# Kernel optimization log

Measured on AMD Instinct MI355X. Metric: run time of the kernel, lower is better.

## Reference

```python
import jax, jax.numpy as jnp
import numpy as np

EPS = 1e-7
MIN_NORM = 1e-15
MAX_NORM = 1e6


def _arcosh(x):
    return jnp.log(x + jnp.sqrt(jnp.clip(x * x - 1.0, EPS, None)))


def _mink_dot(x, y):
    # Minkowski inner product <x,y>_L, keepdim
    return jnp.sum(x * y, axis=-1, keepdims=True) - 2.0 * x[..., 0:1] * y[..., 0:1]


def _mink_norm(u):
    return jnp.sqrt(jnp.clip(_mink_dot(u, u), EPS, None))


def _proj(x, c):
    K = 1.0 / c
    y = x[..., 1:]
    first = jnp.sqrt(jnp.clip(K + jnp.sum(y * y, axis=-1, keepdims=True), EPS, None))
    return jnp.concatenate([first, y], axis=-1)


def _proj_tan(u, x, c):
    ux = jnp.sum(x[..., 1:] * u[..., 1:], axis=-1, keepdims=True)
    first = ux / jnp.clip(x[..., 0:1], EPS, None)
    return jnp.concatenate([first, u[..., 1:]], axis=-1)


def _logmap0(x, c):
    K = 1.0 / c
    sqrtK = jnp.sqrt(K)
    y = x[..., 1:]
    y_norm = jnp.clip(jnp.linalg.norm(y, axis=-1, keepdims=True), MIN_NORM, None)
    theta = jnp.clip(x[..., 0:1] / sqrtK, 1.0 + EPS, None)
    return jnp.concatenate([jnp.zeros_like(theta), sqrtK * _arcosh(theta) * y / y_norm], axis=-1)


def _expmap0(u, c):
    K = 1.0 / c
    sqrtK = jnp.sqrt(K)
    x = u[..., 1:]
    x_norm = jnp.clip(jnp.linalg.norm(x, axis=-1, keepdims=True), MIN_NORM, None)
    theta = x_norm / sqrtK
    return jnp.concatenate([sqrtK * jnp.cosh(theta), sqrtK * jnp.sinh(theta) * x / x_norm], axis=-1)


def _expmap(u, x, c):
    K = 1.0 / c
    sqrtK = jnp.sqrt(K)
    theta = jnp.clip(jnp.clip(_mink_norm(u), None, MAX_NORM) / sqrtK, MIN_NORM, None)
    return _proj(jnp.cosh(theta) * x + jnp.sinh(theta) * u / theta, c)


def _ptransp0(x, u, c):
    K = 1.0 / c
    sqrtK = jnp.sqrt(K)
    x0 = x[..., 0:1]
    y = x[..., 1:]
    y_norm = jnp.clip(jnp.linalg.norm(y, axis=-1, keepdims=True), MIN_NORM, None)
    y_hat = y / y_norm
    v = jnp.concatenate([-y_norm, (sqrtK - x0) * y_hat], axis=-1)
    alpha = jnp.sum(y_hat * u[..., 1:], axis=-1, keepdims=True) / sqrtK
    return _proj_tan(u - alpha * v, x, c)


def _mobius_add(x, y, c):
    u = _logmap0(y, c)
    v = _ptransp0(x, u, c)
    return _expmap(v, x, c)


def _mobius_matvec(m, x, c):
    # rev=False: left-multiply tangent vectors by m
    return _expmap0(m @ _logmap0(x, c), c)


def _sqdist(x, y, c):
    K = 1.0 / c
    theta = jnp.clip(-_mink_dot(x, y) / K, 1.0 + EPS, None)
    return jnp.clip(K * _arcosh(theta) ** 2, None, 50.0)


def _h2k(x):
    return x[..., 1:] / x[..., 0:1]


def _k2h(x):
    sq = jnp.clip(jnp.sum(x * x, axis=-1, keepdims=True), None, 0.999)
    return jnp.concatenate([jnp.ones_like(x[..., 0:1]), x], axis=-1) / jnp.sqrt(1.0 - sq)


def _lorenz_factor(x):
    # default c=1.0 (the learnable c is NOT passed here in the original)
    sq = jnp.clip(jnp.sum(x * x, axis=-1, keepdims=True), None, 0.9)
    return 1.0 / jnp.sqrt(1.0 - sq)


def _one_transform(W, h, b, c):
    n, t, d = h.shape
    # faithful raw row-major reshape (NOT a transpose), matching torch.reshape
    Wh = _mobius_matvec(W, h.reshape(t, n * d), c).reshape(n * t, d)
    return _proj(_mobius_add(Wh, b, c), c)


def setup_inputs() -> dict:
    key = jax.random.key(0)
    n, t, d = 8192, 16, 64
    ks = jax.random.split(key, 3)
    # valid hyperboloid points (c=1): x0 = sqrt(1 + |y|^2)
    y = 0.5 * jax.random.normal(ks[0], (n, t, d - 1), jnp.float32)
    x0 = jnp.sqrt(1.0 + jnp.sum(y * y, axis=-1, keepdims=True))
    big_h = jnp.concatenate([x0, y], axis=-1)
    # all causal time pairs (m, nn<=m) so every segment of the scatter is non-empty
    pairs = np.array([(m, nn) for m in range(t) for nn in range(m + 1)], dtype=np.int64)
    time_index = jnp.asarray(pairs.T)  # (2, 136)
    E = time_index.shape[1]
    mask = jnp.zeros((1, E, 1), jnp.float32)
    lim = float(np.sqrt(6.0 / (t + t)))  # glorot
    w_q = jax.random.uniform(ks[1], (t, t), jnp.float32, -lim, lim)
    w_k = jax.random.uniform(ks[2], (t, t), jnp.float32, -lim, lim)
    b_q = jnp.ones((1, d), jnp.float32)
    b_k = jnp.ones((1, d), jnp.float32)
    a = jnp.ones((1,), jnp.float32)
    c = jnp.ones((1,), jnp.float32)
    return {"big_h": big_h, "time_index": time_index, "mask": mask,
            "w_q": w_q, "w_k": w_k, "b_q": b_q, "b_k": b_k, "a": a, "c": c}


def reference(big_h, time_index, mask, w_q, w_k, b_q, b_k, a, c):
    n, t, d = big_h.shape
    t_m = time_index[0]
    t_n = time_index[1]
    q = _one_transform(w_q, big_h, b_q, c).reshape(n, t, d)
    k = _one_transform(w_k, big_h, b_k, c).reshape(n, t, d)
    v = _h2k(big_h.reshape(n * t, d)).reshape(n, t, d - 1)  # Klein coords
    dist = -_sqdist(q[:, t_m, :], k[:, t_n, :], c)          # (n, E, 1)
    s = jnp.exp(a * dist - c + mask)
    s_sum = jnp.zeros((n, t, 1), s.dtype).at[:, t_m, :].add(s)
    beta = s / s_sum[:, t_n, :]                              # segment softmax
    lamb = _lorenz_factor(v.reshape(n * t, d - 1)).reshape(n, t, 1)[:, t_n, :]
    v_tn = v[:, t_n, :]
    z = v_tn * lamb * beta
    w = lamb * beta
    z_sum = jnp.zeros((n, t, d - 1), z.dtype).at[:, t_m, :].add(z)
    w_sum = jnp.zeros((n, t, 1), w.dtype).at[:, t_m, :].add(w)
    out = z_sum / w_sum                                       # Einstein midpoint
    return _k2h(out.reshape(n * t, d - 1)).reshape(n, t, d)
```

## Files before the change

### kernel.cpp

```cpp
#include <hip/hip_runtime.h>
#include <stdint.h>

typedef unsigned short u16;
typedef unsigned int   u32;

#define EPSF  1e-7f
#define MINN  1e-15f

#define CPR  524288
#define NE   136
#define QS   68
#define VS   68
#define CMS  17
#define NBANK 7

#define WQP 952
#define WKP 1208
#define SCQ 1464
#define SCK 1480
#define CHQ 1496
#define CHK 1512
#define UQ  1528
#define UK  1592

__device__ __forceinline__ float bf2f(u16 u){ u32 x = ((u32)u)<<16; return __uint_as_float(x); }
__device__ __forceinline__ float ldv(const void* p, size_t i, int f32m){
    return f32m ? ((const float*)p)[i] : bf2f(((const u16*)p)[i]);
}
__device__ __forceinline__ float arcosh_f(float x){
    return logf(x + sqrtf(fmaxf(x*x - 1.0f, EPSF)));
}
__device__ __forceinline__ float clampf(float v, float lim){
    return fmaxf(fminf(v, lim), -lim);
}
__device__ __forceinline__ float red16(float v){
    v += __shfl_xor(v,1); v += __shfl_xor(v,2);
    v += __shfl_xor(v,4); v += __shfl_xor(v,8);
    return v;
}
__device__ __forceinline__ int detect_f32(const void* Hv){
    const float* Hf = (const float*)Hv;
    int ok = 1;
#pragma unroll
    for(int i=0;i<16;i++){
        float v = Hf[(size_t)i*1024];
        if(!(v > 0.9f && v < 1000.f)) ok = 0;
    }
    return ok;
}

__device__ __forceinline__ void load_tile(const void* Hv, int f32m, int i0, int c0, float4* hx){
    if(f32m){
        const float* Hf = (const float*)Hv;
#pragma unroll
        for(int s=0;s<16;s++) hx[s] = *(const float4*)(Hf + ((size_t)(512*s + i0))*1024 + c0);
    } else {
        const u16* Hu = (const u16*)Hv;
#pragma unroll
        for(int s=0;s<16;s++){
            ushort4 u4 = *(const ushort4*)(Hu + ((size_t)(512*s + i0))*1024 + c0);
            hx[s] = make_float4(bf2f(u4.x), bf2f(u4.y), bf2f(u4.z), bf2f(u4.w));
        }
    }
}

template<int G>
__device__ __forceinline__ void gram_body(const float4* hx, float* acc){
    int p=0;
#pragma unroll
    for(int s=0;s<16;s++){
#pragma unroll
        for(int s2=s;s2<16;s2++){
            if(p >= 34*G && p < 34*G+34){
                acc[p-34*G] = hx[s].x*hx[s2].x + hx[s].y*hx[s2].y
                            + hx[s].z*hx[s2].z + hx[s].w*hx[s2].w;
            }
            p++;
        }
    }
}

__global__ __launch_bounds__(256) void gram3_k(const void* __restrict__ Hv, float* __restrict__ ws){
    __shared__ float gred[34];
    const int tid = threadIdx.x;
    const int g   = blockIdx.x >> 9;
    const int i0  = blockIdx.x & 511;
    const int f32m = detect_f32(Hv);
    const int c0 = tid*4;

    float4 hx[16];
    load_tile(Hv, f32m, i0, c0, hx);

    float acc[34];
    switch(g){
        case 0: gram_body<0>(hx, acc); break;
        case 1: gram_body<1>(hx, acc); break;
        case 2: gram_body<2>(hx, acc); break;
        default: gram_body<3>(hx, acc); break;
    }

    if(tid<34) gred[tid]=0.f;
    __syncthreads();
#pragma unroll
    for(int j=0;j<34;j++){
        float v=acc[j];
        v+=__shfl_xor(v,1);  v+=__shfl_xor(v,2);  v+=__shfl_xor(v,4);
        v+=__shfl_xor(v,8);  v+=__shfl_xor(v,16); v+=__shfl_xor(v,32);
        if((tid&63)==0) atomicAdd(&gred[j], v);
    }
    __syncthreads();
    if(tid<34) atomicAdd(&ws[(i0%NBANK)*NE + 34*g + tid], gred[tid]);
}

__global__ void fin4_k(const void* __restrict__ Hv, const void* __restrict__ wq, const void* __restrict__ wk,
                       const void* __restrict__ bq, const void* __restrict__ bk, const void* __restrict__ cc,
                       float* __restrict__ ws){
    __shared__ float Gy[16][17], alpha[16], h0s[16], wqp[256], wkp[256], aus[2];
    const int tid = threadIdx.x;
    const int row = tid>>4, l = tid&15;
    const int f32m = detect_f32(Hv);
    float cv = fmaxf(ldv(cc,0,f32m), 1e-20f);
    float K = 1.f/cv, sqK = sqrtf(K);
    if(tid<16) h0s[tid] = ldv(Hv, (size_t)tid*CPR, f32m);
    __syncthreads();
    if(tid<NE){
        int s=0, rem=tid;
        while(rem >= 16 - s){ rem -= 16 - s; s++; }
        int s2 = s + rem;
        float gsum = 0.f;
#pragma unroll
        for(int b=0;b<NBANK;b++) gsum += ws[b*NE+tid];
        float g = gsum - h0s[s]*h0s[s2];
        Gy[s][s2] = g; Gy[s2][s] = g;
    }
    __syncthreads();
    if(tid<16){
        float ny = fmaxf(sqrtf(fmaxf(Gy[tid][tid],0.f)), MINN);
        float th = fmaxf(h0s[tid]/sqK, 1.0f+EPSF);
        alpha[tid] = sqK*arcosh_f(th)/ny;
    }
    __syncthreads();
    {
        float aq = ldv(wq,tid,f32m)*alpha[l];
        float ak = ldv(wk,tid,f32m)*alpha[l];
        wqp[tid] = aq; wkp[tid] = ak;
        ws[WQP+tid] = aq; ws[WKP+tid] = ak;
    }
    if(tid<128){
        int lane = tid&63;
        const void* bb = (tid<64)? bq : bk;
        float v = (lane==0)? 0.f : ldv(bb,lane,f32m);
        float sn = v*v;
        sn += __shfl_xor(sn,1);  sn += __shfl_xor(sn,2);  sn += __shfl_xor(sn,4);
        sn += __shfl_xor(sn,8);  sn += __shfl_xor(sn,16); sn += __shfl_xor(sn,32);
        if(lane==0){
            float b0 = ldv(bb,0,f32m);
            float nb = fmaxf(sqrtf(sn), MINN);
            float th = fmaxf(b0/sqK, 1.0f+EPSF);
            aus[tid>>6] = sqK*arcosh_f(th)/nb;
        }
    }
    __syncthreads();
    {
        float innerQ = 0.f, innerK = 0.f;
#pragma unroll
        for(int s2=0;s2<16;s2++){
            float gy = Gy[l][s2];
            innerQ += wqp[row*16+s2]*gy;
            innerK += wkp[row*16+s2]*gy;
        }
        float tq = red16(wqp[row*16+l]*innerQ);
        float tk = red16(wkp[row*16+l]*innerK);
        if(l==0){
            float xn = fmaxf(sqrtf(fmaxf(tq,0.f)), MINN);
            float thc = fminf(xn/sqK, 80.f);
            ws[SCQ+row] = clampf(sqK*sinhf(thc)/xn, 1e18f);
            ws[CHQ+row] = clampf(sqK*coshf(thc),    1e18f);
            xn = fmaxf(sqrtf(fmaxf(tk,0.f)), MINN);
            thc = fminf(xn/sqK, 80.f);
            ws[SCK+row] = clampf(sqK*sinhf(thc)/xn, 1e18f);
            ws[CHK+row] = clampf(sqK*coshf(thc),    1e18f);
        }
    }
    if(tid<64){
        ws[UQ+tid] = (tid==0)?0.f : clampf(aus[0]*ldv(bq,tid,f32m), 1e18f);
        ws[UK+tid] = (tid==0)?0.f : clampf(aus[1]*ldv(bk,tid,f32m), 1e18f);
    }
}

__global__ __launch_bounds__(256) void main6_k(const void* __restrict__ Hv, const int* __restrict__ tidx,
        const void* __restrict__ mask, const void* __restrict__ aav, const void* __restrict__ ccv,
        const float* __restrict__ ws, float* __restrict__ out){
    __shared__ __attribute__((aligned(16))) float vrow[16*VS];
    __shared__ __attribute__((aligned(16))) float qv[16*QS];
    __shared__ __attribute__((aligned(16))) float kv[16*QS];
    __shared__ float wqp[256], wkp[256], scQ[16], scK[16], chQ[16], chK[16], uq[64], uk[64];
    __shared__ float ssum[16], Cm[16*CMS], lamb[16], invv[16];
    __shared__ int   tmv[NE], tnv[NE];
    __shared__ float maskv[NE];

    const int tid = threadIdx.x;
    const int rb  = blockIdx.x >> 9;
    const int i0  = blockIdx.x & 511;
    const int r0  = rb*2;
    const int row = tid>>4, l = tid&15;
    const int f32m = detect_f32(Hv);
    const float av = ldv(aav,0,f32m);
    const float cv = fmaxf(ldv(ccv,0,f32m), 1e-20f);
    const float K = 1.f/cv, sqK = sqrtf(K);
    const int i64m = (tidx[1] != 1);
    const int c0 = tid*4;

    const float* Hf = (const float*)Hv;
    const u16*   Hu = (const u16*)Hv;

    float4 h0,h1,h2,h3,h4,h5,h6,h7,h8,h9,h10,h11,h12,h13,h14,h15;
    if(f32m){
#define LDF(J, HV) HV = *(const float4*)(Hf + ((size_t)(512*((r0+J)&15) + i0))*1024 + c0);
        LDF(0,h0)  LDF(1,h1)  LDF(2,h2)  LDF(3,h3)
        LDF(4,h4)  LDF(5,h5)  LDF(6,h6)  LDF(7,h7)
        LDF(8,h8)  LDF(9,h9)  LDF(10,h10) LDF(11,h11)
        LDF(12,h12) LDF(13,h13) LDF(14,h14) LDF(15,h15)
#undef LDF
    } else {
#define LDB(J, HV) { ushort4 u4_ = *(const ushort4*)(Hu + ((size_t)(512*((r0+J)&15) + i0))*1024 + c0); \
                     HV = make_float4(bf2f(u4_.x), bf2f(u4_.y), bf2f(u4_.z), bf2f(u4_.w)); }
        LDB(0,h0)  LDB(1,h1)  LDB(2,h2)  LDB(3,h3)
        LDB(4,h4)  LDB(5,h5)  LDB(6,h6)  LDB(7,h7)
        LDB(8,h8)  LDB(9,h9)  LDB(10,h10) LDB(11,h11)
        LDB(12,h12) LDB(13,h13) LDB(14,h14) LDB(15,h15)
#undef LDB
    }

    wqp[tid] = ws[WQP+tid]; wkp[tid] = ws[WKP+tid];
    if(tid<16){ scQ[tid]=ws[SCQ+tid]; scK[tid]=ws[SCK+tid]; chQ[tid]=ws[CHQ+tid]; chK[tid]=ws[CHK+tid]; }
    if(tid<64){ uq[tid]=ws[UQ+tid]; uk[tid]=ws[UK+tid]; }
    if(tid<NE){
        if(i64m){ tmv[tid]=tidx[2*tid]&15; tnv[tid]=tidx[2*NE+2*tid]&15; }
        else    { tmv[tid]=tidx[tid]&15;   tnv[tid]=tidx[NE+tid]&15; }
        maskv[tid]=ldv(mask,tid,f32m);
    }
    __syncthreads();

    auto iter = [&](int r, float4 vr){
        {
            float aq0=0,aq1=0,aq2=0,aq3=0, ak0=0,ak1=0,ak2=0,ak3=0;
#define AFMA(J, HV) { int s_=(r0+J)&15; float wq_=wqp[(r<<4)+s_], wk_=wkp[(r<<4)+s_]; \
            aq0 += wq_*HV.x; aq1 += wq_*HV.y; aq2 += wq_*HV.z; aq3 += wq_*HV.w; \
            ak0 += wk_*HV.x; ak1 += wk_*HV.y; ak2 += wk_*HV.z; ak3 += wk_*HV.w; }
            AFMA(0,h0)  AFMA(1,h1)  AFMA(2,h2)  AFMA(3,h3)
            AFMA(4,h4)  AFMA(5,h5)  AFMA(6,h6)  AFMA(7,h7)
            AFMA(8,h8)  AFMA(9,h9)  AFMA(10,h10) AFMA(11,h11)
            AFMA(12,h12) AFMA(13,h13) AFMA(14,h14) AFMA(15,h15)
#undef AFMA
            float sq_ = scQ[r], sk_ = scK[r];
            float q0 = clampf(sq_*aq0,1e18f), q1=clampf(sq_*aq1,1e18f),
                  q2 = clampf(sq_*aq2,1e18f), q3=clampf(sq_*aq3,1e18f);
            float k0 = clampf(sk_*ak0,1e18f), k1=clampf(sk_*ak1,1e18f),
                  k2 = clampf(sk_*ak2,1e18f), k3=clampf(sk_*ak3,1e18f);
            if(i0==0 && tid==0){ q0 = chQ[r]; k0 = chK[r]; }
            *(float4*)(qv + row*QS + l*4) = make_float4(q0,q1,q2,q3);
            *(float4*)(kv + row*QS + l*4) = make_float4(k0,k1,k2,k3);
        }

        {
            *(float4*)(vrow + row*VS + l*4) = vr;
            float x0v = vrow[row*VS];
            float inv0 = 1.f/((fabsf(x0v)>1e-20f)? x0v : 1e-20f);
            float sv = 0.f;
#pragma unroll
            for(int m=0;m<4;m++){
                int kp = l + 16*m;
                if(kp < 63){ float vi = vrow[row*VS + 1 + kp]*inv0; sv += vi*vi; }
            }
            sv = red16(sv);
            if(l==0){ lamb[row] = 1.f/sqrtf(1.f - fminf(sv, 0.9f)); invv[row] = inv0; }
            if(tid<16) ssum[tid]=0.f;
            Cm[tid]=0.f;
            if(tid<16) Cm[256+tid]=0.f;
        }

        {
            float xq[4], xk[4];
            float syq=0,suq=0,syk=0,suk=0;
#pragma unroll
            for(int m=0;m<4;m++){
                int k = l+16*m;
                xq[m]=qv[row*QS+k]; xk[m]=kv[row*QS+k];
                if(k>0){ syq+=xq[m]*xq[m]; suq+=xq[m]*uq[k];
                         syk+=xk[m]*xk[m]; suk+=xk[m]*uk[k]; }
            }
            syq=red16(syq); suq=red16(suq); syk=red16(syk); suk=red16(suk);
            float x0q=qv[row*QS], x0k=kv[row*QS];
            float xnq=fmaxf(sqrtf(fmaxf(syq,0.f)),MINN);
            float xnk=fmaxf(sqrtf(fmaxf(syk,0.f)),MINN);
            float alq=clampf(suq/(xnq*sqK),1e12f);
            float alk=clampf(suk/(xnk*sqK),1e12f);
            float cfq=clampf(alq*(sqK-x0q)/xnq,1e12f);
            float cfk=clampf(alk*(sqK-x0k)/xnk,1e12f);
            float wq4[4], wk4[4];
            float uxq=0,swq=0,uxk=0,swk=0;
#pragma unroll
            for(int m=0;m<4;m++){
                int k=l+16*m;
                if(k>0){
                    wq4[m]=clampf(uq[k]-cfq*xq[m],1e15f); uxq+=xq[m]*wq4[m]; swq+=wq4[m]*wq4[m];
                    wk4[m]=clampf(uk[k]-cfk*xk[m],1e15f); uxk+=xk[m]*wk4[m]; swk+=wk4[m]*wk4[m];
                } else { wq4[m]=0.f; wk4[m]=0.f; }
            }
            uxq=red16(uxq); swq=red16(swq); uxk=red16(uxk); swk=red16(swk);
            float V0q=uxq/fmaxf(x0q,EPSF);
            float V0k=uxk/fmaxf(x0k,EPSF);
            float mnq=sqrtf(fmaxf(swq-V0q*V0q,EPSF));
            float mnk=sqrtf(fmaxf(swk-V0k*V0k,EPSF));
            float thq=fminf(fmaxf(fminf(mnq,1e6f)/sqK,MINN),20.f);
            float thk=fminf(fmaxf(fminf(mnk,1e6f)/sqK,MINN),20.f);
            float chq=coshf(thq), stq=sinhf(thq)/thq;
            float chk=coshf(thk), stk=sinhf(thk)/thk;
            float zq4[4], zk4[4];
            float szq=0,szk=0;
#pragma unroll
            for(int m=0;m<4;m++){
                int k=l+16*m;
                if(k>0){
                    zq4[m]=clampf(chq*xq[m]+stq*wq4[m],1e15f); szq+=zq4[m]*zq4[m];
                    zk4[m]=clampf(chk*xk[m]+stk*wk4[m],1e15f); szk+=zk4[m]*zk4[m];
                } else { zq4[m]=0.f; zk4[m]=0.f; }
            }
            szq=red16(szq); szk=red16(szk);
            float fq = sqrtf(fmaxf(K+szq,EPSF));
            float fk = sqrtf(fmaxf(K+szk,EPSF));
#pragma unroll
            for(int m=0;m<4;m++){
                int k=l+16*m;
                qv[row*QS+k] = (k==0)? fq : zq4[m];
                kv[row*QS+k] = (k==0)? fk : zk4[m];
            }
        }
        __syncthreads();

        if(tid<NE){
            int m = tmv[tid], nn = tnv[tid];
            const float4* qp = (const float4*)(qv + m*QS);
            const float4* kp = (const float4*)(kv + nn*QS);
            float dot = 0.f;
#pragma unroll
            for(int t4=0;t4<16;t4++){
                float4 q4 = qp[t4], k4 = kp[t4];
                dot += q4.x*k4.x + q4.y*k4.y + q4.z*k4.z + q4.w*k4.w;
            }
            float mdot = dot - 2.f*qv[m*QS]*kv[nn*QS];
            float th = fmaxf(-mdot/K, 1.0f+EPSF);
            float ac = arcosh_f(th);
            float sqd = fminf(K*ac*ac, 50.f);
            float sval = expf(fminf(-av*sqd - cv + maskv[tid], 80.f));
            Cm[m*CMS+nn] = sval;
            atomicAdd(&ssum[m], sval);
        }
        __syncthreads();

        if(tid<NE){
            int m = tmv[tid], nn = tnv[tid];
            Cm[m*CMS+nn] = lamb[nn]*Cm[m*CMS+nn]/fmaxf(ssum[nn],1e-37f);
        }
        __syncthreads();

        {
            float cs[16]; float wsm = 0.f;
#pragma unroll
            for(int s=0;s<16;s++){
                float cmv = Cm[row*CMS+s];
                wsm += cmv;
                cs[s] = cmv*invv[s];
            }
            wsm = fmaxf(wsm, 1e-37f);
            float g4[4]; float sg=0.f;
#pragma unroll
            for(int m=0;m<4;m++){
                int kp = l+16*m;
                float num = 0.f;
#pragma unroll
                for(int s=0;s<16;s++) num += cs[s]*vrow[s*VS + 1 + kp];
                float gvv = (kp<63)? num/wsm : 0.f;
                g4[m]=gvv; sg += gvv*gvv;
            }
            sg = red16(sg);
            float inv = 1.f/sqrtf(1.f - fminf(sg, 0.999f));
            size_t base = ((size_t)(512*r + i0)*16 + row)*64;
            if(l==0) out[base] = inv;
#pragma unroll
            for(int m=0;m<4;m++){
                int kp=l+16*m;
                if(kp<63) out[base+1+kp] = g4[m]*inv;
            }
        }
        __syncthreads();
    };

    iter(r0+0, h0);
    iter(r0+1, h1);
}

extern "C" void kernel_launch(void* const* d_in, const int* in_sizes, int n_in,
                              void* d_out, int out_size, void* d_ws, size_t ws_size,
                              hipStream_t stream){
    const void* H    = d_in[0];
    const int* tidx  = (const int*)d_in[1];
    const void* mask = d_in[2];
    const void* wq   = d_in[3];
    const void* wk   = d_in[4];
    const void* bq   = d_in[5];
    const void* bk   = d_in[6];
    const void* aa   = d_in[7];
    const void* cc   = d_in[8];
    float* out = (float*)d_out;
    float* ws  = (float*)d_ws;

    hipMemsetAsync(ws, 0, NBANK*NE*sizeof(float), stream);
    gram3_k<<<2048,256,0,stream>>>(H, ws);
    fin4_k <<<1,   256,0,stream>>>(H, wq, wk, bq, bk, cc, ws);
    main6_k<<<4096,256,0,stream>>>(H, tidx, mask, aa, cc, ws, out);
}
```

Before: 212.1 us.

## Process one row per block, streaming H loads instead of register caching

```diff
diff --git a/kernel.cpp b/kernel.cpp
--- a/kernel.cpp
+++ b/kernel.cpp
@@ -188,7 +188,7 @@
     }
 }
 
-__global__ __launch_bounds__(256) void main6_k(const void* __restrict__ Hv, const int* __restrict__ tidx,
+__global__ __launch_bounds__(256,6) void main7_k(const void* __restrict__ Hv, const int* __restrict__ tidx,
         const void* __restrict__ mask, const void* __restrict__ aav, const void* __restrict__ ccv,
         const float* __restrict__ ws, float* __restrict__ out){
     __shared__ __attribute__((aligned(16))) float vrow[16*VS];
@@ -200,9 +200,8 @@
     __shared__ float maskv[NE];
 
     const int tid = threadIdx.x;
-    const int rb  = blockIdx.x >> 9;
+    const int r   = blockIdx.x >> 9;
     const int i0  = blockIdx.x & 511;
-    const int r0  = rb*2;
     const int row = tid>>4, l = tid&15;
     const int f32m = detect_f32(Hv);
     const float av = ldv(aav,0,f32m);
@@ -214,24 +213,6 @@
     const float* Hf = (const float*)Hv;
     const u16*   Hu = (const u16*)Hv;
 
-    float4 h0,h1,h2,h3,h4,h5,h6,h7,h8,h9,h10,h11,h12,h13,h14,h15;
-    if(f32m){
-#define LDF(J, HV) HV = *(const float4*)(Hf + ((size_t)(512*((r0+J)&15) + i0))*1024 + c0);
-        LDF(0,h0)  LDF(1,h1)  LDF(2,h2)  LDF(3,h3)
-        LDF(4,h4)  LDF(5,h5)  LDF(6,h6)  LDF(7,h7)
-        LDF(8,h8)  LDF(9,h9)  LDF(10,h10) LDF(11,h11)
-        LDF(12,h12) LDF(13,h13) LDF(14,h14) LDF(15,h15)
-#undef LDF
-    } else {
-#define LDB(J, HV) { ushort4 u4_ = *(const ushort4*)(Hu + ((size_t)(512*((r0+J)&15) + i0))*1024 + c0); \
-                     HV = make_float4(bf2f(u4_.x), bf2f(u4_.y), bf2f(u4_.z), bf2f(u4_.w)); }
-        LDB(0,h0)  LDB(1,h1)  LDB(2,h2)  LDB(3,h3)
-        LDB(4,h4)  LDB(5,h5)  LDB(6,h6)  LDB(7,h7)
-        LDB(8,h8)  LDB(9,h9)  LDB(10,h10) LDB(11,h11)
-        LDB(12,h12) LDB(13,h13) LDB(14,h14) LDB(15,h15)
-#undef LDB
-    }
-
     wqp[tid] = ws[WQP+tid]; wkp[tid] = ws[WKP+tid];
     if(tid<16){ scQ[tid]=ws[SCQ+tid]; scK[tid]=ws[SCK+tid]; chQ[tid]=ws[CHQ+tid]; chK[tid]=ws[CHK+tid]; }
     if(tid<64){ uq[tid]=ws[UQ+tid]; uk[tid]=ws[UK+tid]; }
@@ -242,163 +223,178 @@
     }
     __syncthreads();
 
-    auto iter = [&](int r, float4 vr){
-        {
-            float aq0=0,aq1=0,aq2=0,aq3=0, ak0=0,ak1=0,ak2=0,ak3=0;
-#define AFMA(J, HV) { int s_=(r0+J)&15; float wq_=wqp[(r<<4)+s_], wk_=wkp[(r<<4)+s_]; \
-            aq0 += wq_*HV.x; aq1 += wq_*HV.y; aq2 += wq_*HV.z; aq3 += wq_*HV.w; \
-            ak0 += wk_*HV.x; ak1 += wk_*HV.y; ak2 += wk_*HV.z; ak3 += wk_*HV.w; }
-            AFMA(0,h0)  AFMA(1,h1)  AFMA(2,h2)  AFMA(3,h3)
-            AFMA(4,h4)  AFMA(5,h5)  AFMA(6,h6)  AFMA(7,h7)
-            AFMA(8,h8)  AFMA(9,h9)  AFMA(10,h10) AFMA(11,h11)
-            AFMA(12,h12) AFMA(13,h13) AFMA(14,h14) AFMA(15,h15)
-#undef AFMA
-            float sq_ = scQ[r], sk_ = scK[r];
-            float q0 = clampf(sq_*aq0,1e18f), q1=clampf(sq_*aq1,1e18f),
-                  q2 = clampf(sq_*aq2,1e18f), q3=clampf(sq_*aq3,1e18f);
-            float k0 = clampf(sk_*ak0,1e18f), k1=clampf(sk_*ak1,1e18f),
-                  k2 = clampf(sk_*ak2,1e18f), k3=clampf(sk_*ak3,1e18f);
-            if(i0==0 && tid==0){ q0 = chQ[r]; k0 = chK[r]; }
-            *(float4*)(qv + row*QS + l*4) = make_float4(q0,q1,q2,q3);
-            *(float4*)(kv + row*QS + l*4) = make_float4(k0,k1,k2,k3);
-        }
-
-        {
-            *(float4*)(vrow + row*VS + l*4) = vr;
-            float x0v = vrow[row*VS];
-            float inv0 = 1.f/((fabsf(x0v)>1e-20f)? x0v : 1e-20f);
-            float sv = 0.f;
-#pragma unroll
-            for(int m=0;m<4;m++){
-                int kp = l + 16*m;
-                if(kp < 63){ float vi = vrow[row*VS + 1 + kp]*inv0; sv += vi*vi; }
-            }
-            sv = red16(sv);
-            if(l==0){ lamb[row] = 1.f/sqrtf(1.f - fminf(sv, 0.9f)); invv[row] = inv0; }
-            if(tid<16) ssum[tid]=0.f;
-            Cm[tid]=0.f;
-            if(tid<16) Cm[256+tid]=0.f;
-        }
-
-        {
-            float xq[4], xk[4];
-            float syq=0,suq=0,syk=0,suk=0;
-#pragma unroll
-            for(int m=0;m<4;m++){
-                int k = l+16*m;
-                xq[m]=qv[row*QS+k]; xk[m]=kv[row*QS+k];
-                if(k>0){ syq+=xq[m]*xq[m]; suq+=xq[m]*uq[k];
-                         syk+=xk[m]*xk[m]; suk+=xk[m]*uk[k]; }
-            }
-            syq=red16(syq); suq=red16(suq); syk=red16(syk); suk=red16(suk);
-            float x0q=qv[row*QS], x0k=kv[row*QS];
-            float xnq=fmaxf(sqrtf(fmaxf(syq,0.f)),MINN);
-            float xnk=fmaxf(sqrtf(fmaxf(syk,0.f)),MINN);
-            float alq=clampf(suq/(xnq*sqK),1e12f);
-            float alk=clampf(suk/(xnk*sqK),1e12f);
-            float cfq=clampf(alq*(sqK-x0q)/xnq,1e12f);
-            float cfk=clampf(alk*(sqK-x0k)/xnk,1e12f);
-            float wq4[4], wk4[4];
-            float uxq=0,swq=0,uxk=0,swk=0;
-#pragma unroll
-            for(int m=0;m<4;m++){
-                int k=l+16*m;
-                if(k>0){
-                    wq4[m]=clampf(uq[k]-cfq*xq[m],1e15f); uxq+=xq[m]*wq4[m]; swq+=wq4[m]*wq4[m];
-                    wk4[m]=clampf(uk[k]-cfk*xk[m],1e15f); uxk+=xk[m]*wk4[m]; swk+=wk4[m]*wk4[m];
-                } else { wq4[m]=0.f; wk4[m]=0.f; }
-            }
-            uxq=red16(uxq); swq=red16(swq); uxk=red16(uxk); swk=red16(swk);
-            float V0q=uxq/fmaxf(x0q,EPSF);
-            float V0k=uxk/fmaxf(x0k,EPSF);
-            float mnq=sqrtf(fmaxf(swq-V0q*V0q,EPSF));
-            float mnk=sqrtf(fmaxf(swk-V0k*V0k,EPSF));
-            float thq=fminf(fmaxf(fminf(mnq,1e6f)/sqK,MINN),20.f);
-            float thk=fminf(fmaxf(fminf(mnk,1e6f)/sqK,MINN),20.f);
-            float chq=coshf(thq), stq=sinhf(thq)/thq;
-            float chk=coshf(thk), stk=sinhf(thk)/thk;
-            float zq4[4], zk4[4];
-            float szq=0,szk=0;
-#pragma unroll
-            for(int m=0;m<4;m++){
-                int k=l+16*m;
-                if(k>0){
-                    zq4[m]=clampf(chq*xq[m]+stq*wq4[m],1e15f); szq+=zq4[m]*zq4[m];
-                    zk4[m]=clampf(chk*xk[m]+stk*wk4[m],1e15f); szk+=zk4[m]*zk4[m];
-                } else { zq4[m]=0.f; zk4[m]=0.f; }
-            }
-            szq=red16(szq); szk=red16(szk);
-            float fq = sqrtf(fmaxf(K+szq,EPSF));
-            float fk = sqrtf(fmaxf(K+szk,EPSF));
-#pragma unroll
-            for(int m=0;m<4;m++){
-                int k=l+16*m;
-                qv[row*QS+k] = (k==0)? fq : zq4[m];
-                kv[row*QS+k] = (k==0)? fk : zk4[m];
-            }
-        }
-        __syncthreads();
-
-        if(tid<NE){
-            int m = tmv[tid], nn = tnv[tid];
-            const float4* qp = (const float4*)(qv + m*QS);
-            const float4* kp = (const float4*)(kv + nn*QS);
-            float dot = 0.f;
-#pragma unroll
-            for(int t4=0;t4<16;t4++){
-                float4 q4 = qp[t4], k4 = kp[t4];
-                dot += q4.x*k4.x + q4.y*k4.y + q4.z*k4.z + q4.w*k4.w;
-            }
-            float mdot = dot - 2.f*qv[m*QS]*kv[nn*QS];
-            float th = fmaxf(-mdot/K, 1.0f+EPSF);
-            float ac = arcosh_f(th);
-            float sqd = fminf(K*ac*ac, 50.f);
-            float sval = expf(fminf(-av*sqd - cv + maskv[tid], 80.f));
-            Cm[m*CMS+nn] = sval;
-            atomicAdd(&ssum[m], sval);
-        }
-        __syncthreads();
-
-        if(tid<NE){
-            int m = tmv[tid], nn = tnv[tid];
-            Cm[m*CMS+nn] = lamb[nn]*Cm[m*CMS+nn]/fmaxf(ssum[nn],1e-37f);
-        }
-        __syncthreads();
-
-        {
-            float cs[16]; float wsm = 0.f;
-#pragma unroll
-            for(int s=0;s<16;s++){
-                float cmv = Cm[row*CMS+s];
-                wsm += cmv;
-                cs[s] = cmv*invv[s];
-            }
-            wsm = fmaxf(wsm, 1e-37f);
-            float g4[4]; float sg=0.f;
-#pragma unroll
-            for(int m=0;m<4;m++){
-                int kp = l+16*m;
-                float num = 0.f;
-#pragma unroll
-                for(int s=0;s<16;s++) num += cs[s]*vrow[s*VS + 1 + kp];
-                float gvv = (kp<63)? num/wsm : 0.f;
-                g4[m]=gvv; sg += gvv*gvv;
-            }
-            sg = red16(sg);
-            float inv = 1.f/sqrtf(1.f - fminf(sg, 0.999f));
-            size_t base = ((size_t)(512*r + i0)*16 + row)*64;
-            if(l==0) out[base] = inv;
-#pragma unroll
-            for(int m=0;m<4;m++){
-                int kp=l+16*m;
-                if(kp<63) out[base+1+kp] = g4[m]*inv;
-            }
-        }
-        __syncthreads();
-    };
-
-    iter(r0+0, h0);
-    iter(r0+1, h1);
+    float aq0=0,aq1=0,aq2=0,aq3=0, ak0=0,ak1=0,ak2=0,ak3=0;
+    float4 vr;
+    const int rQ = r<<4;
+    if(f32m){
+#define STEPF(J) { const int s_=(r+J)&15; \
+        float4 b = *(const float4*)(Hf + ((size_t)(512*s_ + i0))*1024 + c0); \
+        if(J==0) vr = b; \
+        float wq_=wqp[rQ+s_], wk_=wkp[rQ+s_]; \
+        aq0 += wq_*b.x; aq1 += wq_*b.y; aq2 += wq_*b.z; aq3 += wq_*b.w; \
+        ak0 += wk_*b.x; ak1 += wk_*b.y; ak2 += wk_*b.z; ak3 += wk_*b.w; }
+        STEPF(0)  STEPF(1)  STEPF(2)  STEPF(3)
+        STEPF(4)  STEPF(5)  STEPF(6)  STEPF(7)
+        STEPF(8)  STEPF(9)  STEPF(10) STEPF(11)
+        STEPF(12) STEPF(13) STEPF(14) STEPF(15)
+#undef STEPF
+    } else {
+#define STEPB(J) { const int s_=(r+J)&15; \
+        ushort4 u4_ = *(const ushort4*)(Hu + ((size_t)(512*s_ + i0))*1024 + c0); \
+        float4 b = make_float4(bf2f(u4_.x), bf2f(u4_.y), bf2f(u4_.z), bf2f(u4_.w)); \
+        if(J==0) vr = b; \
+        float wq_=wqp[rQ+s_], wk_=wkp[rQ+s_]; \
+        aq0 += wq_*b.x; aq1 += wq_*b.y; aq2 += wq_*b.z; aq3 += wq_*b.w; \
+        ak0 += wk_*b.x; ak1 += wk_*b.y; ak2 += wk_*b.z; ak3 += wk_*b.w; }
+        STEPB(0)  STEPB(1)  STEPB(2)  STEPB(3)
+        STEPB(4)  STEPB(5)  STEPB(6)  STEPB(7)
+        STEPB(8)  STEPB(9)  STEPB(10) STEPB(11)
+        STEPB(12) STEPB(13) STEPB(14) STEPB(15)
+#undef STEPB
+    }
+
+    {
+        float sq_ = scQ[r], sk_ = scK[r];
+        float q0 = clampf(sq_*aq0,1e18f), q1=clampf(sq_*aq1,1e18f),
+              q2 = clampf(sq_*aq2,1e18f), q3=clampf(sq_*aq3,1e18f);
+        float k0 = clampf(sk_*ak0,1e18f), k1=clampf(sk_*ak1,1e18f),
+              k2 = clampf(sk_*ak2,1e18f), k3=clampf(sk_*ak3,1e18f);
+        if(i0==0 && tid==0){ q0 = chQ[r]; k0 = chK[r]; }
+        *(float4*)(qv + row*QS + l*4) = make_float4(q0,q1,q2,q3);
+        *(float4*)(kv + row*QS + l*4) = make_float4(k0,k1,k2,k3);
+    }
+
+    {
+        *(float4*)(vrow + row*VS + l*4) = vr;
+        float x0v = vrow[row*VS];
+        float inv0 = 1.f/((fabsf(x0v)>1e-20f)? x0v : 1e-20f);
+        float sv = 0.f;
+#pragma unroll
+        for(int m=0;m<4;m++){
+            int kp = l + 16*m;
+            if(kp < 63){ float vi = vrow[row*VS + 1 + kp]*inv0; sv += vi*vi; }
+        }
+        sv = red16(sv);
+        if(l==0){ lamb[row] = 1.f/sqrtf(1.f - fminf(sv, 0.9f)); invv[row] = inv0; }
+        if(tid<16) ssum[tid]=0.f;
+        Cm[tid]=0.f;
+        if(tid<16) Cm[256+tid]=0.f;
+    }
+
+    {
+        float xq[4], xk[4];
+        float syq=0,suq=0,syk=0,suk=0;
+#pragma unroll
+        for(int m=0;m<4;m++){
+            int k = l+16*m;
+            xq[m]=qv[row*QS+k]; xk[m]=kv[row*QS+k];
+            if(k>0){ syq+=xq[m]*xq[m]; suq+=xq[m]*uq[k];
+                     syk+=xk[m]*xk[m]; suk+=xk[m]*uk[k]; }
+        }
+        syq=red16(syq); suq=red16(suq); syk=red16(syk); suk=red16(suk);
+        float x0q=qv[row*QS], x0k=kv[row*QS];
+        float xnq=fmaxf(sqrtf(fmaxf(syq,0.f)),MINN);
+        float xnk=fmaxf(sqrtf(fmaxf(syk,0.f)),MINN);
+        float alq=clampf(suq/(xnq*sqK),1e12f);
+        float alk=clampf(suk/(xnk*sqK),1e12f);
+        float cfq=clampf(alq*(sqK-x0q)/xnq,1e12f);
+        float cfk=clampf(alk*(sqK-x0k)/xnk,1e12f);
+        float wq4[4], wk4[4];
+        float uxq=0,swq=0,uxk=0,swk=0;
+#pragma unroll
+        for(int m=0;m<4;m++){
+            int k=l+16*m;
+            if(k>0){
+                wq4[m]=clampf(uq[k]-cfq*xq[m],1e15f); uxq+=xq[m]*wq4[m]; swq+=wq4[m]*wq4[m];
+                wk4[m]=clampf(uk[k]-cfk*xk[m],1e15f); uxk+=xk[m]*wk4[m]; swk+=wk4[m]*wk4[m];
+            } else { wq4[m]=0.f; wk4[m]=0.f; }
+        }
+        uxq=red16(uxq); swq=red16(swq); uxk=red16(uxk); swk=red16(swk);
+        float V0q=uxq/fmaxf(x0q,EPSF);
+        float V0k=uxk/fmaxf(x0k,EPSF);
+        float mnq=sqrtf(fmaxf(swq-V0q*V0q,EPSF));
+        float mnk=sqrtf(fmaxf(swk-V0k*V0k,EPSF));
+        float thq=fminf(fmaxf(fminf(mnq,1e6f)/sqK,MINN),20.f);
+        float thk=fminf(fmaxf(fminf(mnk,1e6f)/sqK,MINN),20.f);
+        float chq=coshf(thq), stq=sinhf(thq)/thq;
+        float chk=coshf(thk), stk=sinhf(thk)/thk;
+        float zq4[4], zk4[4];
+        float szq=0,szk=0;
+#pragma unroll
+        for(int m=0;m<4;m++){
+            int k=l+16*m;
+            if(k>0){
+                zq4[m]=clampf(chq*xq[m]+stq*wq4[m],1e15f); szq+=zq4[m]*zq4[m];
+                zk4[m]=clampf(chk*xk[m]+stk*wk4[m],1e15f); szk+=zk4[m]*zk4[m];
+            } else { zq4[m]=0.f; zk4[m]=0.f; }
+        }
+        szq=red16(szq); szk=red16(szk);
+        float fq = sqrtf(fmaxf(K+szq,EPSF));
+        float fk = sqrtf(fmaxf(K+szk,EPSF));
+#pragma unroll
+        for(int m=0;m<4;m++){
+            int k=l+16*m;
+            qv[row*QS+k] = (k==0)? fq : zq4[m];
+            kv[row*QS+k] = (k==0)? fk : zk4[m];
+        }
+    }
+    __syncthreads();
+
+    if(tid<NE){
+        int m = tmv[tid], nn = tnv[tid];
+        const float4* qp = (const float4*)(qv + m*QS);
+        const float4* kp = (const float4*)(kv + nn*QS);
+        float dot = 0.f;
+#pragma unroll
+        for(int t4=0;t4<16;t4++){
+            float4 q4 = qp[t4], k4 = kp[t4];
+            dot += q4.x*k4.x + q4.y*k4.y + q4.z*k4.z + q4.w*k4.w;
+        }
+        float mdot = dot - 2.f*qv[m*QS]*kv[nn*QS];
+        float th = fmaxf(-mdot/K, 1.0f+EPSF);
+        float ac = arcosh_f(th);
+        float sqd = fminf(K*ac*ac, 50.f);
+        float sval = expf(fminf(-av*sqd - cv + maskv[tid], 80.f));
+        Cm[m*CMS+nn] = sval;
+        atomicAdd(&ssum[m], sval);
+    }
+    __syncthreads();
+
+    if(tid<NE){
+        int m = tmv[tid], nn = tnv[tid];
+        Cm[m*CMS+nn] = lamb[nn]*Cm[m*CMS+nn]/fmaxf(ssum[nn],1e-37f);
+    }
+    __syncthreads();
+
+    {
+        float cs[16]; float wsm = 0.f;
+#pragma unroll
+        for(int s=0;s<16;s++){
+            float cmv = Cm[row*CMS+s];
+            wsm += cmv;
+            cs[s] = cmv*invv[s];
+        }
+        wsm = fmaxf(wsm, 1e-37f);
+        float g4[4]; float sg=0.f;
+#pragma unroll
+        for(int m=0;m<4;m++){
+            int kp = l+16*m;
+            float num = 0.f;
+#pragma unroll
+            for(int s=0;s<16;s++) num += cs[s]*vrow[s*VS + 1 + kp];
+            float gvv = (kp<63)? num/wsm : 0.f;
+            g4[m]=gvv; sg += gvv*gvv;
+        }
+        sg = red16(sg);
+        float inv = 1.f/sqrtf(1.f - fminf(sg, 0.999f));
+        size_t base = ((size_t)(512*r + i0)*16 + row)*64;
+        if(l==0) out[base] = inv;
+#pragma unroll
+        for(int m=0;m<4;m++){
+            int kp=l+16*m;
+            if(kp<63) out[base+1+kp] = g4[m]*inv;
+        }
+    }
 }
 
 extern "C" void kernel_launch(void* const* d_in, const int* in_sizes, int n_in,
@@ -419,5 +415,5 @@
     hipMemsetAsync(ws, 0, NBANK*NE*sizeof(float), stream);
     gram3_k<<<2048,256,0,stream>>>(H, ws);
     fin4_k <<<1,   256,0,stream>>>(H, wq, wk, bq, bk, cc, ws);
-    main6_k<<<4096,256,0,stream>>>(H, tidx, mask, aa, cc, ws, out);
-}
+    main7_k<<<8192,256,0,stream>>>(H, tidx, mask, aa, cc, ws, out);
+}
```

New measurement: 194.6 us. 8.3% less time.
